# Performance work log

Measured on AMD Instinct MI355X. Metric: run time of the kernel, lower is better.

Reference implementation:

```python
import jax, jax.numpy as jnp
import numpy as np

B, N, F_IN = 1, 4096, 128
H, F_OUT = 8, 64
NEG = -1e9


def setup_inputs() -> dict:
    key = jax.random.key(0)
    ks = jax.random.split(key, 7)
    x = jax.random.normal(ks[0], (B, N, F_IN), dtype=jnp.float32)
    edge = jax.random.uniform(ks[1], (N, N)) < 0.02
    edge = edge | jnp.eye(N, dtype=bool)
    adj = jnp.where(edge, 0.0, NEG).astype(jnp.float32)
    # Glorot-uniform params
    def glorot(k, shape, fan_in, fan_out):
        lim = float(np.sqrt(6.0 / (fan_in + fan_out)))
        return jax.random.uniform(k, shape, jnp.float32, -lim, lim)
    W_proj = glorot(ks[2], (H * F_OUT, F_IN), F_IN, H * F_OUT)      # linear_proj.weight
    a_src = glorot(ks[3], (1, H, F_OUT), H, F_OUT)                   # scoring_fn_source
    a_tgt = glorot(ks[4], (1, H, F_OUT), H, F_OUT)                   # scoring_fn_target
    W_skip = glorot(ks[5], (H * F_OUT, F_IN), F_IN, H * F_OUT)       # skip_proj.weight
    bias = jnp.zeros((H * F_OUT,), dtype=jnp.float32)
    return {"in_nodes_features": x, "adj": adj, "W_proj": W_proj,
            "a_src": a_src, "a_tgt": a_tgt, "W_skip": W_skip, "bias": bias}


def reference(in_nodes_features, adj, W_proj, a_src, a_tgt, W_skip, bias):
    x = in_nodes_features                                  # [B,N,Fin]  (dropout p=0)
    proj = jnp.einsum('bnf,of->bno', x, W_proj)            # [B,N,H*Fo]
    proj = proj.reshape(B, N, H, F_OUT)                    # [B,N,H,Fo]
    s_src = jnp.einsum('bnhd,xhd->bhn', proj, a_src)       # [B,H,N] (row / source)
    s_tgt = jnp.einsum('bnhd,xhd->bhn', proj, a_tgt)       # [B,H,N] (col / target)
    scores = s_src[:, :, :, None] + s_tgt[:, :, None, :]   # [B,H,N,N]
    scores = jax.nn.leaky_relu(scores, negative_slope=0.2)
    att = jax.nn.softmax(scores + adj, axis=-1)            # adj additive mask, broadcast over B,H
    out = jnp.einsum('bhij,bjhd->bihd', att, proj)         # [B,N,H,Fo]
    out = out + jnp.einsum('bnf,of->bno', x, W_skip).reshape(B, N, H, F_OUT)  # skip (dims differ)
    out = out.reshape(B, N, H * F_OUT) + bias              # concat + bias
    out = jax.nn.elu(out)                                  # activation ELU
    return out, adj
```

## Files before the change

kernel.cpp:

```cpp
#include <hip/hip_runtime.h>
#include <cmath>

#define N_NODES 4096
#define FIN     128
#define H_HEADS 8
#define FOUT    64
#define HF      512
#define CAP     256

typedef float  vf4 __attribute__((ext_vector_type(4)));
typedef float  vf2 __attribute__((ext_vector_type(2)));
typedef unsigned int vu4 __attribute__((ext_vector_type(4)));

__device__ __forceinline__ unsigned short f2bf(float f) {
    unsigned u = __float_as_uint(f);
    u += 0x7fff + ((u >> 16) & 1);
    return (unsigned short)(u >> 16);
}

__global__ __launch_bounds__(256) void k1_fused(
    const float* __restrict__ x, const float* __restrict__ Wp,
    const float* __restrict__ Ws, const float* __restrict__ a_src,
    const float* __restrict__ a_tgt, const float* __restrict__ adj,
    unsigned short* __restrict__ proj, float* __restrict__ skip,
    float* __restrict__ ssrc, float* __restrict__ stgt,
    int* __restrict__ cnt, int* __restrict__ idx,
    float* __restrict__ adj_out)
{
    __shared__ __align__(16) float smem[2 * 32 * 68];
    const int bx = blockIdx.x;
    const int t  = threadIdx.x;
    const int q5 = bx / 5;

    if (bx - q5 * 5 == 0) {
        const int g  = q5;
        float (*AsT)[68] = (float(*)[68])smem;
        float (*BsT)[68] = (float(*)[68])(smem + 32 * 68);
        const int rb = (g >> 4) * 64;
        const int cb = (g & 15) * 64;
        const bool isP = (cb < HF);
        const float* Wbase = isP ? (Wp + cb * FIN) : (Ws + (cb - HF) * FIN);

        const int tx = t & 15;
        const int ty = t >> 4;
        float acc[4][4] = {{0.f}};

        for (int kb = 0; kb < FIN; kb += 32) {
            #pragma unroll
            for (int p = 0; p < 2; ++p) {
                int f4 = t + p * 256;
                int r  = f4 >> 3;
                int k4 = f4 & 7;
                float4 a = *(const float4*)(x + (size_t)(rb + r) * FIN + kb + k4 * 4);
                AsT[k4*4+0][r] = a.x; AsT[k4*4+1][r] = a.y;
                AsT[k4*4+2][r] = a.z; AsT[k4*4+3][r] = a.w;
                float4 b = *(const float4*)(Wbase + (size_t)r * FIN + kb + k4 * 4);
                BsT[k4*4+0][r] = b.x; BsT[k4*4+1][r] = b.y;
                BsT[k4*4+2][r] = b.z; BsT[k4*4+3][r] = b.w;
            }
            __syncthreads();
            #pragma unroll 8
            for (int kk = 0; kk < 32; ++kk) {
                float4 a = *(const float4*)&AsT[kk][ty * 4];
                float4 b = *(const float4*)&BsT[kk][tx * 4];
                acc[0][0] += a.x*b.x; acc[0][1] += a.x*b.y; acc[0][2] += a.x*b.z; acc[0][3] += a.x*b.w;
                acc[1][0] += a.y*b.x; acc[1][1] += a.y*b.y; acc[1][2] += a.y*b.z; acc[1][3] += a.y*b.w;
                acc[2][0] += a.z*b.x; acc[2][1] += a.z*b.y; acc[2][2] += a.z*b.z; acc[2][3] += a.z*b.w;
                acc[3][0] += a.w*b.x; acc[3][1] += a.w*b.y; acc[3][2] += a.w*b.z; acc[3][3] += a.w*b.w;
            }
            __syncthreads();
        }

        if (isP) {
            #pragma unroll
            for (int i = 0; i < 4; ++i) {
                ushort4 v;
                v.x = f2bf(acc[i][0]); v.y = f2bf(acc[i][1]);
                v.z = f2bf(acc[i][2]); v.w = f2bf(acc[i][3]);
                *(ushort4*)(proj + (size_t)(rb + ty*4 + i) * HF + cb + tx * 4) = v;
            }
            const int h = cb >> 6;
            const float as0 = a_src[cb + tx*4 + 0], as1 = a_src[cb + tx*4 + 1];
            const float as2 = a_src[cb + tx*4 + 2], as3 = a_src[cb + tx*4 + 3];
            const float at0 = a_tgt[cb + tx*4 + 0], at1 = a_tgt[cb + tx*4 + 1];
            const float at2 = a_tgt[cb + tx*4 + 2], at3 = a_tgt[cb + tx*4 + 3];
            #pragma unroll
            for (int i = 0; i < 4; ++i) {
                float ps = acc[i][0]*as0 + acc[i][1]*as1 + acc[i][2]*as2 + acc[i][3]*as3;
                float pt = acc[i][0]*at0 + acc[i][1]*at1 + acc[i][2]*at2 + acc[i][3]*at3;
                #pragma unroll
                for (int off = 1; off < 16; off <<= 1) {
                    ps += __shfl_xor(ps, off);
                    pt += __shfl_xor(pt, off);
                }
                if (tx == 0) {
                    int n = rb + ty*4 + i;
                    ssrc[n * H_HEADS + h] = ps;
                    stgt[n * H_HEADS + h] = pt;
                }
            }
        } else {
            #pragma unroll
            for (int i = 0; i < 4; ++i) {
                float4 v = make_float4(acc[i][0], acc[i][1], acc[i][2], acc[i][3]);
                *(float4*)(skip + (size_t)(rb + ty*4 + i) * HF + (cb - HF) + tx * 4) = v;
            }
        }
    } else {
        __shared__ int lcnt;
        const int i    = bx - q5 - 1;
        const int lane = t & 63;
        if (t == 0) lcnt = 0;
        __syncthreads();
        const unsigned long long lt = (1ull << lane) - 1ull;
        const vf4* arow = (const vf4*)(adj + (size_t)i * N_NODES);
        vf4*       aout = (vf4*)(adj_out + (size_t)i * N_NODES);
        int* rowidx = idx + i * CAP;
        #pragma unroll
        for (int it = 0; it < 4; ++it) {
            const int f4 = t + it * 256;
            vf4 v = __builtin_nontemporal_load(arow + f4);
            __builtin_nontemporal_store(v, aout + f4);
            const int jb = (f4 * 4) << 10;
            const bool h0 = (v.x == 0.f), h1 = (v.y == 0.f), h2 = (v.z == 0.f), h3 = (v.w == 0.f);
            const unsigned long long b0 = __ballot(h0), b1 = __ballot(h1);
            const unsigned long long b2 = __ballot(h2), b3 = __ballot(h3);
            const int n0 = __popcll(b0), n1 = __popcll(b1), n2 = __popcll(b2);
            const int total = n0 + n1 + n2 + __popcll(b3);
            int base = 0;
            if (lane == 0 && total) base = atomicAdd(&lcnt, total);
            base = __shfl(base, 0);
            if (h0) { int p = base + __popcll(b0 & lt);                if (p < CAP) rowidx[p] = jb;        }
            if (h1) { int p = base + n0 + __popcll(b1 & lt);           if (p < CAP) rowidx[p] = jb + 1024; }
            if (h2) { int p = base + n0 + n1 + __popcll(b2 & lt);      if (p < CAP) rowidx[p] = jb + 2048; }
            if (h3) { int p = base + n0 + n1 + n2 + __popcll(b3 & lt); if (p < CAP) rowidx[p] = jb + 3072; }
        }
        __syncthreads();
        if (t == 0) cnt[i] = lcnt;
    }
}

__global__ __launch_bounds__(256, 8) void att_kernel(
    const unsigned short* __restrict__ proj, const float* __restrict__ skip,
    const float* __restrict__ ssrc, const float* __restrict__ stgt,
    const float* __restrict__ bias, const int* __restrict__ cnt,
    const int* __restrict__ idx, float* __restrict__ out)
{
    __shared__ int   s_idx[CAP];
    __shared__ float sp[4][CAP];
    __shared__ float s_i[4];

    const int t    = threadIdx.x;
    const int i    = blockIdx.x >> 1;
    const int hb   = (blockIdx.x & 1) * 4;
    const int lane = t & 63;
    if (t < 4) s_i[t] = ssrc[i * H_HEADS + hb + t];
    int c = cnt[i]; if (c > CAP) c = CAP;
    __syncthreads();

    for (int k = t; k < c; k += 256) {
        const int off = idx[i * CAP + k];
        s_idx[k] = off;
        const float4 t0 = *(const float4*)((const char*)stgt + (off >> 5) + hb * 4);
        float e;
        e = s_i[0] + t0.x; sp[0][k] = (e > 0.f) ? e : 0.2f * e;
        e = s_i[1] + t0.y; sp[1][k] = (e > 0.f) ? e : 0.2f * e;
        e = s_i[2] + t0.z; sp[2][k] = (e > 0.f) ? e : 0.2f * e;
        e = s_i[3] + t0.w; sp[3][k] = (e > 0.f) ? e : 0.2f * e;
    }
    __syncthreads();

    const int w = t >> 6;
    float m = -1e30f;
    for (int k = lane; k < c; k += 64) m = fmaxf(m, sp[w][k]);
    #pragma unroll
    for (int off = 32; off; off >>= 1) m = fmaxf(m, __shfl_xor(m, off));
    float l = 0.0f;
    for (int k = lane; k < c; k += 64) {
        float e = __expf(sp[w][k] - m);
        sp[w][k] = e;
        l += e;
    }
    #pragma unroll
    for (int off = 32; off; off >>= 1) l += __shfl_xor(l, off);
    const float inv = 1.0f / l;

    const int g  = lane >> 3;
    const int k8 = lane & 7;
    vf2 a2[4] = {{0.f, 0.f}, {0.f, 0.f}, {0.f, 0.f}, {0.f, 0.f}};
    const char* pbase = (const char*)proj + (hb + w) * FOUT * 2 + k8 * 16;
    int k = g;
    for (; k + 24 < c; k += 32) {
        const int o0 = s_idx[k], o1 = s_idx[k + 8], o2 = s_idx[k + 16], o3 = s_idx[k + 24];
        vu4 r0 = *(const vu4*)(pbase + o0);
        vu4 r1 = *(const vu4*)(pbase + o1);
        vu4 r2 = *(const vu4*)(pbase + o2);
        vu4 r3 = *(const vu4*)(pbase + o3);
        const float p0 = sp[w][k], p1 = sp[w][k + 8], p2 = sp[w][k + 16], p3 = sp[w][k + 24];
        const vf2 q0 = {p0, p0}, q1 = {p1, p1}, q2 = {p2, p2}, q3 = {p3, p3};
        a2[0] += q0 * (vf2){ __uint_as_float(r0.x << 16), __uint_as_float(r0.x & 0xffff0000u) };
        a2[1] += q0 * (vf2){ __uint_as_float(r0.y << 16), __uint_as_float(r0.y & 0xffff0000u) };
        a2[2] += q0 * (vf2){ __uint_as_float(r0.z << 16), __uint_as_float(r0.z & 0xffff0000u) };
        a2[3] += q0 * (vf2){ __uint_as_float(r0.w << 16), __uint_as_float(r0.w & 0xffff0000u) };
        a2[0] += q1 * (vf2){ __uint_as_float(r1.x << 16), __uint_as_float(r1.x & 0xffff0000u) };
        a2[1] += q1 * (vf2){ __uint_as_float(r1.y << 16), __uint_as_float(r1.y & 0xffff0000u) };
        a2[2] += q1 * (vf2){ __uint_as_float(r1.z << 16), __uint_as_float(r1.z & 0xffff0000u) };
        a2[3] += q1 * (vf2){ __uint_as_float(r1.w << 16), __uint_as_float(r1.w & 0xffff0000u) };
        a2[0] += q2 * (vf2){ __uint_as_float(r2.x << 16), __uint_as_float(r2.x & 0xffff0000u) };
        a2[1] += q2 * (vf2){ __uint_as_float(r2.y << 16), __uint_as_float(r2.y & 0xffff0000u) };
        a2[2] += q2 * (vf2){ __uint_as_float(r2.z << 16), __uint_as_float(r2.z & 0xffff0000u) };
        a2[3] += q2 * (vf2){ __uint_as_float(r2.w << 16), __uint_as_float(r2.w & 0xffff0000u) };
        a2[0] += q3 * (vf2){ __uint_as_float(r3.x << 16), __uint_as_float(r3.x & 0xffff0000u) };
        a2[1] += q3 * (vf2){ __uint_as_float(r3.y << 16), __uint_as_float(r3.y & 0xffff0000u) };
        a2[2] += q3 * (vf2){ __uint_as_float(r3.z << 16), __uint_as_float(r3.z & 0xffff0000u) };
        a2[3] += q3 * (vf2){ __uint_as_float(r3.w << 16), __uint_as_float(r3.w & 0xffff0000u) };
    }
    for (; k < c; k += 8) {
        const int   off = s_idx[k];
        const float p   = sp[w][k];
        const vf2   p2  = {p, p};
        vu4 raw = *(const vu4*)(pbase + off);
        a2[0] += p2 * (vf2){ __uint_as_float(raw.x << 16), __uint_as_float(raw.x & 0xffff0000u) };
        a2[1] += p2 * (vf2){ __uint_as_float(raw.y << 16), __uint_as_float(raw.y & 0xffff0000u) };
        a2[2] += p2 * (vf2){ __uint_as_float(raw.z << 16), __uint_as_float(raw.z & 0xffff0000u) };
        a2[3] += p2 * (vf2){ __uint_as_float(raw.w << 16), __uint_as_float(raw.w & 0xffff0000u) };
    }
    float a8[8] = {a2[0].x, a2[0].y, a2[1].x, a2[1].y,
                   a2[2].x, a2[2].y, a2[3].x, a2[3].y};
    #pragma unroll
    for (int off = 8; off < 64; off <<= 1) {
        #pragma unroll
        for (int q = 0; q < 8; ++q) a8[q] += __shfl_xor(a8[q], off);
    }
    if (g == 0) {
        const int o = (hb + w) * FOUT + k8 * 8;
        const float* sk = skip + (size_t)i * HF + o;
        const float* bs = bias + o;
        float r[8];
        #pragma unroll
        for (int q = 0; q < 8; ++q) {
            float v = a8[q] * inv + sk[q] + bs[q];
            r[q] = (v > 0.f) ? v : expm1f(v);
        }
        *(float4*)(out + (size_t)i * HF + o)     = make_float4(r[0], r[1], r[2], r[3]);
        *(float4*)(out + (size_t)i * HF + o + 4) = make_float4(r[4], r[5], r[6], r[7]);
    }
}

extern "C" void kernel_launch(void* const* d_in, const int* in_sizes, int n_in,
                              void* d_out, int out_size, void* d_ws, size_t ws_size,
                              hipStream_t stream)
{
    const float* x     = (const float*)d_in[0];
    const float* adj   = (const float*)d_in[1];
    const float* Wp    = (const float*)d_in[2];
    const float* a_src = (const float*)d_in[3];
    const float* a_tgt = (const float*)d_in[4];
    const float* Ws    = (const float*)d_in[5];
    const float* bias  = (const float*)d_in[6];

    float* out     = (float*)d_out;
    float* adj_out = out + (size_t)N_NODES * HF;

    unsigned short* proj = (unsigned short*)d_ws;
    float* ssrc = (float*)((char*)d_ws + (size_t)N_NODES * HF * 2);
    float* stgt = ssrc + (size_t)N_NODES * H_HEADS;
    int*   cnt  = (int*)(stgt + (size_t)N_NODES * H_HEADS);
    int*   idxb = cnt + N_NODES;
    float* skip = out;

    k1_fused<<<1024 + N_NODES, 256, 0, stream>>>(
        x, Wp, Ws, a_src, a_tgt, adj, proj, skip, ssrc, stgt, cnt, idxb, adj_out);
    att_kernel<<<2 * N_NODES, 256, 0, stream>>>(proj, skip, ssrc, stgt, bias,
                                                cnt, idxb, out);
}
```

Measured before the change: 188.8 us.

## Split adjacency row scan across two blocks with global atomic counters

Each adjacency row is now scanned by two blocks, each handling half the row, instead of one. Per-row neighbor counts are accumulated with global atomics into a counter array that a memset clears before the launch, and the shared-memory counter and its barriers are removed. The GEMM blocks are moved to the front of the grid instead of being interleaved every fifth block, and the adjacency load is no longer nontemporal. This aims to raise parallelism and shorten the scan tail. It costs an extra memset launch, and neighbor index order within a row becomes nondeterministic.

```diff
diff --git a/kernel.cpp b/kernel.cpp
--- a/kernel.cpp
+++ b/kernel.cpp
@@ -7,6 +7,8 @@
 #define FOUT    64
 #define HF      512
 #define CAP     256
+#define GEMM_BLOCKS 1024
+#define ADJ_SPLIT 2
 
 typedef float  vf4 __attribute__((ext_vector_type(4)));
 typedef float  vf2 __attribute__((ext_vector_type(2)));
@@ -30,14 +32,12 @@
     __shared__ __align__(16) float smem[2 * 32 * 68];
     const int bx = blockIdx.x;
     const int t  = threadIdx.x;
-    const int q5 = bx / 5;
-
-    if (bx - q5 * 5 == 0) {
-        const int g  = q5;
+
+    if (bx < GEMM_BLOCKS) {
         float (*AsT)[68] = (float(*)[68])smem;
         float (*BsT)[68] = (float(*)[68])(smem + 32 * 68);
-        const int rb = (g >> 4) * 64;
-        const int cb = (g & 15) * 64;
+        const int rb = (bx >> 4) * 64;
+        const int cb = (bx & 15) * 64;
         const bool isP = (cb < HF);
         const float* Wbase = isP ? (Wp + cb * FIN) : (Ws + (cb - HF) * FIN);
 
@@ -107,36 +107,34 @@
             }
         }
     } else {
-        __shared__ int lcnt;
-        const int i    = bx - q5 - 1;
+        const int job  = bx - GEMM_BLOCKS;
+        const int i    = job >> 1;
+        const int half = job & 1;
         const int lane = t & 63;
-        if (t == 0) lcnt = 0;
-        __syncthreads();
         const unsigned long long lt = (1ull << lane) - 1ull;
-        const vf4* arow = (const vf4*)(adj + (size_t)i * N_NODES);
-        vf4*       aout = (vf4*)(adj_out + (size_t)i * N_NODES);
+        const int base4 = half * 512;
+        const vf4* arow = (const vf4*)(adj + (size_t)i * N_NODES) + base4;
+        vf4*       aout = (vf4*)(adj_out + (size_t)i * N_NODES) + base4;
         int* rowidx = idx + i * CAP;
         #pragma unroll
-        for (int it = 0; it < 4; ++it) {
+        for (int it = 0; it < 2; ++it) {
             const int f4 = t + it * 256;
-            vf4 v = __builtin_nontemporal_load(arow + f4);
+            vf4 v = arow[f4];
             __builtin_nontemporal_store(v, aout + f4);
-            const int jb = (f4 * 4) << 10;
+            const int jb = ((base4 + f4) * 4) << 10;
             const bool h0 = (v.x == 0.f), h1 = (v.y == 0.f), h2 = (v.z == 0.f), h3 = (v.w == 0.f);
             const unsigned long long b0 = __ballot(h0), b1 = __ballot(h1);
             const unsigned long long b2 = __ballot(h2), b3 = __ballot(h3);
             const int n0 = __popcll(b0), n1 = __popcll(b1), n2 = __popcll(b2);
             const int total = n0 + n1 + n2 + __popcll(b3);
             int base = 0;
-            if (lane == 0 && total) base = atomicAdd(&lcnt, total);
+            if (lane == 0 && total) base = atomicAdd(&cnt[i], total);
             base = __shfl(base, 0);
             if (h0) { int p = base + __popcll(b0 & lt);                if (p < CAP) rowidx[p] = jb;        }
             if (h1) { int p = base + n0 + __popcll(b1 & lt);           if (p < CAP) rowidx[p] = jb + 1024; }
             if (h2) { int p = base + n0 + n1 + __popcll(b2 & lt);      if (p < CAP) rowidx[p] = jb + 2048; }
             if (h3) { int p = base + n0 + n1 + n2 + __popcll(b3 & lt); if (p < CAP) rowidx[p] = jb + 3072; }
         }
-        __syncthreads();
-        if (t == 0) cnt[i] = lcnt;
     }
 }
 
@@ -269,7 +267,8 @@
     int*   idxb = cnt + N_NODES;
     float* skip = out;
 
-    k1_fused<<<1024 + N_NODES, 256, 0, stream>>>(
+    hipMemsetAsync(cnt, 0, N_NODES * sizeof(int), stream);
+    k1_fused<<<GEMM_BLOCKS + ADJ_SPLIT * N_NODES, 256, 0, stream>>>(
         x, Wp, Ws, a_src, a_tgt, adj, proj, skip, ssrc, stgt, cnt, idxb, adj_out);
     att_kernel<<<2 * N_NODES, 256, 0, stream>>>(proj, skip, ssrc, stgt, bias,
                                                 cnt, idxb, out);
```

Result: no change. 189.3 us (+0.3%).
